# Kernel tuning notes

Measured on AMD Instinct MI355X. Metric: run time of the kernel, lower is better.

## Reference

```python
import jax, jax.numpy as jnp
import numpy as np

B = 256
K = 16          # NUM_MIXTURES
BINS = (128, 128)
RANGE = (-2.0, 2.0, -2.0, 2.0)
MIN_SIGMA = 0.001


def setup_inputs() -> dict:
    key = jax.random.key(0)
    k1, k2, k3, k4 = jax.random.split(key, 4)
    mu = jax.random.normal(k1, (B, K, 2), dtype=jnp.float32)
    sigma = jax.random.uniform(k2, (B, K, 2), dtype=jnp.float32)
    cov12 = jax.random.normal(k3, (B, K), dtype=jnp.float32)
    pi = jax.random.uniform(k4, (B, K), dtype=jnp.float32)
    return {"mu": mu, "sigma": sigma, "cov12": cov12, "pi": pi}


def reference(mu, sigma, cov12, pi):
    # gmm_to_hist: splat B*K 2x2 Gaussians onto a 128x128 grid, vectorized
    u = jnp.linspace(RANGE[0], RANGE[1], BINS[0])
    v = jnp.linspace(RANGE[2], RANGE[3], BINS[1])
    uu, vv = jnp.meshgrid(u, v, indexing='ij')
    gu = uu.reshape(-1)  # [G]
    gv = vv.reshape(-1)  # [G]

    sigma = jnp.maximum(sigma, MIN_SIGMA)
    su2 = sigma[..., 0] ** 2  # [B,K]
    sv2 = sigma[..., 1] ** 2
    c11 = su2 + 1e-6
    c22 = sv2 + 1e-6
    off = cov12

    det_full = c11 * c22 - off ** 2
    valid = (det_full > 0) & ~jnp.isnan(det_full)
    det_safe = jnp.where(valid, det_full, 1.0)  # avoid div-by-bad-det in dead branch

    # closed-form 2x2 inverse; fallback = diag(clamped sigma^2) as in torch code
    ia = jnp.where(valid, c22 / det_safe, 1.0 / su2)   # inv[0,0]
    ib = jnp.where(valid, -off / det_safe, 0.0)        # inv[0,1]
    ic = jnp.where(valid, c11 / det_safe, 1.0 / sv2)   # inv[1,1]
    det = jnp.where(valid, det_full, su2 * sv2)

    du = gu[None, None, :] - mu[..., 0:1]  # [B,K,G]
    dv = gv[None, None, :] - mu[..., 1:2]  # [B,K,G]
    mahal = ia[..., None] * du * du + 2.0 * ib[..., None] * du * dv + ic[..., None] * dv * dv

    coef = pi / (2.0 * jnp.pi * jnp.sqrt(det + 1e-6))  # [B,K]
    hist = jnp.einsum('bk,bkg->bg', coef, jnp.exp(-0.5 * mahal))  # sum over mixtures
    hist = hist.reshape(-1, BINS[0], BINS[1])

    s = hist.sum(axis=(1, 2), keepdims=True)
    hist = hist / jnp.where(s > 0, s, 1.0)
    return hist
```

## Files before the change

### kernel.cpp

```cpp
#include <hip/hip_runtime.h>
#include <math.h>

#define BB   256
#define KK   16
#define NBIN 128
#define GG   (NBIN * NBIN)
#define NT   1024
#define SPT  (GG / NT)

__device__ __forceinline__ float raw_exp2(float x) {
#if __has_builtin(__builtin_amdgcn_exp2f)
    return __builtin_amdgcn_exp2f(x);
#else
    float r;
    asm volatile("v_exp_f32 %0, %1\n\ts_nop 1" : "=v"(r) : "v"(x));
    return r;
#endif
}

__global__ __launch_bounds__(NT) void gmm_hist_kernel(
    const float* __restrict__ mu,
    const float* __restrict__ sigma,
    const float* __restrict__ cov12,
    const float* __restrict__ pi_,
    float* __restrict__ out)
{
    const int b   = blockIdx.x;
    const int tid = threadIdx.x;

    __shared__ float4 s_par[2 * KK];
    __shared__ float  s_wsum[NT / 64];
    __shared__ float  s_total;

    if (tid < KK) {
        const int idx = b * KK + tid;
        const float m_u = mu[idx * 2 + 0];
        const float m_v = mu[idx * 2 + 1];
        const float su  = fmaxf(sigma[idx * 2 + 0], 0.001f);
        const float sv  = fmaxf(sigma[idx * 2 + 1], 0.001f);
        const float su2 = su * su;
        const float sv2 = sv * sv;
        const float c11 = su2 + 1e-6f;
        const float c22 = sv2 + 1e-6f;
        const float off = cov12[idx];
        const float det_full = c11 * c22 - off * off;
        const bool  valid    = (det_full > 0.0f);
        const float det_safe = valid ? det_full : 1.0f;
        const float ia  = valid ? (c22 / det_safe) : (1.0f / su2);
        const float ib  = valid ? (-off / det_safe) : 0.0f;
        const float ic  = valid ? (c11 / det_safe) : (1.0f / sv2);
        const float det = valid ? det_full : (su2 * sv2);
        const float coef = pi_[idx] / (6.283185307179586f * sqrtf(det + 1e-6f));
        const float cs = -0.7213475204444817f;
        s_par[2 * tid + 0] = make_float4(m_u, m_v, ia * cs, (2.0f * ib) * cs);
        s_par[2 * tid + 1] = make_float4(ic * cs, coef, 0.0f, 0.0f);
    }
    __syncthreads();

    const float step = 4.0f / 127.0f;
    const int   j    = tid & (NBIN - 1);
    const int   i0   = tid >> 7;
    const float gv   = -2.0f + (float)j * step;
    const float u0   = -2.0f + (float)i0 * step;

    float acc[SPT];
    #pragma unroll
    for (int s = 0; s < SPT; ++s) acc[s] = 0.0f;

    #pragma unroll
    for (int k = 0; k < KK; ++k) {
        const float4 p0 = s_par[2 * k + 0];
        const float4 p1 = s_par[2 * k + 1];
        const float dv   = gv - p0.y;
        const float ia   = p0.z;
        const float Bp   = p0.w * dv;
        const float Ap   = p1.x * (dv * dv);
        const float coef = p1.y;
        const float base = u0 - p0.x;

        #pragma unroll
        for (int h = 0; h < SPT; h += 8) {
            float m8[8];
            #pragma unroll
            for (int t = 0; t < 8; ++t) {
                const float du = base + (float)(8 * (h + t)) * step;
                const float tt = __builtin_fmaf(ia, du, Bp);
                m8[t] = __builtin_fmaf(du, tt, Ap);
            }
            float e8[8];
            #pragma unroll
            for (int t = 0; t < 8; ++t) e8[t] = raw_exp2(m8[t]);
            #pragma unroll
            for (int t = 0; t < 8; ++t)
                acc[h + t] = __builtin_fmaf(coef, e8[t], acc[h + t]);
        }
    }

    float local = 0.0f;
    #pragma unroll
    for (int s = 0; s < SPT; ++s) local += acc[s];

    #pragma unroll
    for (int off = 32; off >= 1; off >>= 1)
        local += __shfl_down(local, off, 64);

    const int wave = tid >> 6;
    const int lane = tid & 63;
    if (lane == 0) s_wsum[wave] = local;
    __syncthreads();

    if (tid == 0) {
        float t = 0.0f;
        #pragma unroll
        for (int w = 0; w < NT / 64; ++w) t += s_wsum[w];
        s_total = (t > 0.0f) ? t : 1.0f;
    }
    __syncthreads();

    const float inv = 1.0f / s_total;
    float* outb = out + (size_t)b * GG;
    #pragma unroll
    for (int s = 0; s < SPT; ++s)
        outb[s * NT + tid] = acc[s] * inv;
}

extern "C" void kernel_launch(void* const* d_in, const int* in_sizes, int n_in,
                              void* d_out, int out_size, void* d_ws, size_t ws_size,
                              hipStream_t stream) {
    const float* mu    = (const float*)d_in[0];
    const float* sigma = (const float*)d_in[1];
    const float* cov12 = (const float*)d_in[2];
    const float* pi_   = (const float*)d_in[3];
    float* out = (float*)d_out;

    hipLaunchKernelGGL(gmm_hist_kernel, dim3(BB), dim3(NT), 0, stream,
                       mu, sigma, cov12, pi_, out);
}
```

Before: 76.77 us.

## Split each batch histogram across eight blocks with a separate normalize pass

```diff
diff --git a/kernel.cpp b/kernel.cpp
--- a/kernel.cpp
+++ b/kernel.cpp
@@ -1,12 +1,14 @@
 #include <hip/hip_runtime.h>
 #include <math.h>
 
-#define BB   256
-#define KK   16
-#define NBIN 128
-#define GG   (NBIN * NBIN)
-#define NT   1024
-#define SPT  (GG / NT)
+#define BB     256
+#define KK     16
+#define NBIN   128
+#define GG     (NBIN * NBIN)
+#define SLICES 8
+#define NT1    256
+#define SPT    8
+#define NT2    256
 
 __device__ __forceinline__ float raw_exp2(float x) {
 #if __has_builtin(__builtin_amdgcn_exp2f)
@@ -18,19 +20,21 @@
 #endif
 }
 
-__global__ __launch_bounds__(NT) void gmm_hist_kernel(
+__global__ __launch_bounds__(NT1, 8) void gmm_hist_partial(
     const float* __restrict__ mu,
     const float* __restrict__ sigma,
     const float* __restrict__ cov12,
     const float* __restrict__ pi_,
-    float* __restrict__ out)
+    float* __restrict__ out,
+    float* __restrict__ psum)
 {
-    const int b   = blockIdx.x;
+    const int bb  = blockIdx.x;
+    const int b   = bb >> 3;
+    const int p   = bb & 7;
     const int tid = threadIdx.x;
 
     __shared__ float4 s_par[2 * KK];
-    __shared__ float  s_wsum[NT / 64];
-    __shared__ float  s_total;
+    __shared__ float  s_wsum[NT1 / 64];
 
     if (tid < KK) {
         const int idx = b * KK + tid;
@@ -58,70 +62,83 @@
     __syncthreads();
 
     const float step = 4.0f / 127.0f;
-    const int   j    = tid & (NBIN - 1);
-    const int   i0   = tid >> 7;
-    const float gv   = -2.0f + (float)j * step;
-    const float u0   = -2.0f + (float)i0 * step;
+    const int   i    = (p << 4) + (tid >> 4);
+    const int   j0   = (tid & 15) << 3;
+    const float ui   = -2.0f + (float)i  * step;
+    const float v0   = -2.0f + (float)j0 * step;
 
     float acc[SPT];
     #pragma unroll
-    for (int s = 0; s < SPT; ++s) acc[s] = 0.0f;
+    for (int e = 0; e < SPT; ++e) acc[e] = 0.0f;
 
     #pragma unroll
     for (int k = 0; k < KK; ++k) {
-        const float4 p0 = s_par[2 * k + 0];
-        const float4 p1 = s_par[2 * k + 1];
-        const float dv   = gv - p0.y;
-        const float ia   = p0.z;
-        const float Bp   = p0.w * dv;
-        const float Ap   = p1.x * (dv * dv);
-        const float coef = p1.y;
-        const float base = u0 - p0.x;
+        const float4 q0 = s_par[2 * k + 0];
+        const float4 q1 = s_par[2 * k + 1];
+        const float du   = ui - q0.x;
+        const float dvb  = v0 - q0.y;
+        const float C2   = q1.x;
+        const float C1   = q0.w * du;
+        const float C0   = (q0.z * du) * du;
+        const float coef = q1.y;
 
+        float m8[SPT];
         #pragma unroll
-        for (int h = 0; h < SPT; h += 8) {
-            float m8[8];
-            #pragma unroll
-            for (int t = 0; t < 8; ++t) {
-                const float du = base + (float)(8 * (h + t)) * step;
-                const float tt = __builtin_fmaf(ia, du, Bp);
-                m8[t] = __builtin_fmaf(du, tt, Ap);
-            }
-            float e8[8];
-            #pragma unroll
-            for (int t = 0; t < 8; ++t) e8[t] = raw_exp2(m8[t]);
-            #pragma unroll
-            for (int t = 0; t < 8; ++t)
-                acc[h + t] = __builtin_fmaf(coef, e8[t], acc[h + t]);
+        for (int e = 0; e < SPT; ++e) {
+            const float dv = dvb + (float)e * step;
+            m8[e] = __builtin_fmaf(dv, __builtin_fmaf(C2, dv, C1), C0);
         }
+        float e8[SPT];
+        #pragma unroll
+        for (int e = 0; e < SPT; ++e) e8[e] = raw_exp2(m8[e]);
+        #pragma unroll
+        for (int e = 0; e < SPT; ++e)
+            acc[e] = __builtin_fmaf(coef, e8[e], acc[e]);
     }
 
     float local = 0.0f;
     #pragma unroll
-    for (int s = 0; s < SPT; ++s) local += acc[s];
-
+    for (int e = 0; e < SPT; ++e) local += acc[e];
     #pragma unroll
     for (int off = 32; off >= 1; off >>= 1)
         local += __shfl_down(local, off, 64);
-
     const int wave = tid >> 6;
     const int lane = tid & 63;
     if (lane == 0) s_wsum[wave] = local;
     __syncthreads();
-
     if (tid == 0) {
         float t = 0.0f;
         #pragma unroll
-        for (int w = 0; w < NT / 64; ++w) t += s_wsum[w];
-        s_total = (t > 0.0f) ? t : 1.0f;
+        for (int w = 0; w < NT1 / 64; ++w) t += s_wsum[w];
+        psum[bb] = t;
     }
-    __syncthreads();
 
-    const float inv = 1.0f / s_total;
-    float* outb = out + (size_t)b * GG;
+    float4* o4 = reinterpret_cast<float4*>(out + (size_t)b * GG + ((size_t)p << 11));
+    o4[2 * tid + 0] = make_float4(acc[0], acc[1], acc[2], acc[3]);
+    o4[2 * tid + 1] = make_float4(acc[4], acc[5], acc[6], acc[7]);
+}
+
+__global__ __launch_bounds__(NT2) void gmm_hist_norm(
+    const float* __restrict__ psum,
+    float* __restrict__ out)
+{
+    const int bb  = blockIdx.x;
+    const int b   = bb >> 3;
+    const int p   = bb & 7;
+    const int tid = threadIdx.x;
+
+    float t = 0.0f;
     #pragma unroll
-    for (int s = 0; s < SPT; ++s)
-        outb[s * NT + tid] = acc[s] * inv;
+    for (int r = 0; r < SLICES; ++r) t += psum[b * SLICES + r];
+    const float inv = (t > 0.0f) ? (1.0f / t) : 1.0f;
+
+    float4* o4 = reinterpret_cast<float4*>(out + (size_t)b * GG + ((size_t)p << 11));
+    float4 a = o4[tid];
+    float4 c = o4[tid + NT2];
+    a.x *= inv; a.y *= inv; a.z *= inv; a.w *= inv;
+    c.x *= inv; c.y *= inv; c.z *= inv; c.w *= inv;
+    o4[tid]       = a;
+    o4[tid + NT2] = c;
 }
 
 extern "C" void kernel_launch(void* const* d_in, const int* in_sizes, int n_in,
@@ -131,8 +148,11 @@
     const float* sigma = (const float*)d_in[1];
     const float* cov12 = (const float*)d_in[2];
     const float* pi_   = (const float*)d_in[3];
-    float* out = (float*)d_out;
+    float* out  = (float*)d_out;
+    float* psum = (float*)d_ws;
 
-    hipLaunchKernelGGL(gmm_hist_kernel, dim3(BB), dim3(NT), 0, stream,
-                       mu, sigma, cov12, pi_, out);
+    hipLaunchKernelGGL(gmm_hist_partial, dim3(BB * SLICES), dim3(NT1), 0, stream,
+                       mu, sigma, cov12, pi_, out, psum);
+    hipLaunchKernelGGL(gmm_hist_norm, dim3(BB * SLICES), dim3(NT2), 0, stream,
+                       psum, out);
 }
```

New measurement: 90.60 us. 18.0% more time.

## Skip negligible Gaussian components per wave using eigenvalue bound and remap pixels

Applied to the files above, without the earlier changes.

```diff
diff --git a/kernel.cpp b/kernel.cpp
--- a/kernel.cpp
+++ b/kernel.cpp
@@ -7,6 +7,7 @@
 #define GG   (NBIN * NBIN)
 #define NT   1024
 #define SPT  (GG / NT)
+
 
 __device__ __forceinline__ float raw_exp2(float x) {
 #if __has_builtin(__builtin_amdgcn_exp2f)
@@ -52,53 +53,65 @@
         const float det = valid ? det_full : (su2 * sv2);
         const float coef = pi_[idx] / (6.283185307179586f * sqrtf(det + 1e-6f));
         const float cs = -0.7213475204444817f;
+
+        const float lh   = 0.5f * (ia + ic);
+        const float lq   = sqrtf(0.25f * (ia - ic) * (ia - ic) + ib * ib);
+        const float lmin = fmaxf(lh - lq, 0.0f);
+        const float L    = lmin * cs;
+        const float dv0  = fmaxf(fabsf(m_v) - 2.0f, 0.0f);
+
         s_par[2 * tid + 0] = make_float4(m_u, m_v, ia * cs, (2.0f * ib) * cs);
-        s_par[2 * tid + 1] = make_float4(ic * cs, coef, 0.0f, 0.0f);
+        s_par[2 * tid + 1] = make_float4(ic * cs, coef, L, L * dv0 * dv0);
     }
     __syncthreads();
 
     const float step = 4.0f / 127.0f;
-    const int   j    = tid & (NBIN - 1);
-    const int   i0   = tid >> 7;
-    const float gv   = -2.0f + (float)j * step;
-    const float u0   = -2.0f + (float)i0 * step;
+    const int   r    = tid >> 3;
+    const int   c0   = (tid & 7) << 4;
+    const float gu   = -2.0f + (float)r  * step;
+    const float v0   = -2.0f + (float)c0 * step;
 
     float acc[SPT];
     #pragma unroll
-    for (int s = 0; s < SPT; ++s) acc[s] = 0.0f;
+    for (int e = 0; e < SPT; ++e) acc[e] = 0.0f;
 
     #pragma unroll
     for (int k = 0; k < KK; ++k) {
         const float4 p0 = s_par[2 * k + 0];
         const float4 p1 = s_par[2 * k + 1];
-        const float dv   = gv - p0.y;
-        const float ia   = p0.z;
-        const float Bp   = p0.w * dv;
-        const float Ap   = p1.x * (dv * dv);
-        const float coef = p1.y;
-        const float base = u0 - p0.x;
+        const float du   = gu - p0.x;
+        const float du2  = du * du;
 
-        #pragma unroll
-        for (int h = 0; h < SPT; h += 8) {
-            float m8[8];
+        const float bound = __builtin_fmaf(p1.z, du2, p1.w);
+        if (__any(bound > -46.0f)) {
+            const float dvb  = v0 - p0.y;
+            const float C2   = p1.x;
+            const float C1   = p0.w * du;
+            const float C0   = p0.z * du2;
+            const float coef = p1.y;
+
             #pragma unroll
-            for (int t = 0; t < 8; ++t) {
-                const float du = base + (float)(8 * (h + t)) * step;
-                const float tt = __builtin_fmaf(ia, du, Bp);
-                m8[t] = __builtin_fmaf(du, tt, Ap);
+            for (int h = 0; h < SPT; h += 8) {
+                float m8[8];
+                #pragma unroll
+                for (int t = 0; t < 8; ++t) {
+                    const float dv = dvb + (float)(h + t) * step;
+                    const float tt = __builtin_fmaf(C2, dv, C1);
+                    m8[t] = __builtin_fmaf(dv, tt, C0);
+                }
+                float e8[8];
+                #pragma unroll
+                for (int t = 0; t < 8; ++t) e8[t] = raw_exp2(m8[t]);
+                #pragma unroll
+                for (int t = 0; t < 8; ++t)
+                    acc[h + t] = __builtin_fmaf(coef, e8[t], acc[h + t]);
             }
-            float e8[8];
-            #pragma unroll
-            for (int t = 0; t < 8; ++t) e8[t] = raw_exp2(m8[t]);
-            #pragma unroll
-            for (int t = 0; t < 8; ++t)
-                acc[h + t] = __builtin_fmaf(coef, e8[t], acc[h + t]);
         }
     }
 
     float local = 0.0f;
     #pragma unroll
-    for (int s = 0; s < SPT; ++s) local += acc[s];
+    for (int e = 0; e < SPT; ++e) local += acc[e];
 
     #pragma unroll
     for (int off = 32; off >= 1; off >>= 1)
@@ -118,10 +131,11 @@
     __syncthreads();
 
     const float inv = 1.0f / s_total;
-    float* outb = out + (size_t)b * GG;
+    float4* o4 = reinterpret_cast<float4*>(out + (size_t)b * GG + (size_t)tid * SPT);
     #pragma unroll
-    for (int s = 0; s < SPT; ++s)
-        outb[s * NT + tid] = acc[s] * inv;
+    for (int q = 0; q < SPT / 4; ++q)
+        o4[q] = make_float4(acc[4 * q + 0] * inv, acc[4 * q + 1] * inv,
+                            acc[4 * q + 2] * inv, acc[4 * q + 3] * inv);
 }
 
 extern "C" void kernel_launch(void* const* d_in, const int* in_sizes, int n_in,
```

Result: slower. 79.97 us (+4.2%).
